# Optimization experiments

Hardware: AMD Instinct MI355X
Metric: run time of the kernel (lower is better)

The kernel has to match this reference:

```python
import jax, jax.numpy as jnp
import numpy as np

H = 8          # n_heads
THRESH = 0.5   # edge pruning threshold
LN_EPS = 1e-5


def setup_inputs() -> dict:
    key = jax.random.key(0)
    ks = jax.random.split(key, 24)
    B, S, D = 8, 128, 256
    N = S + 1
    hd = D // H

    def lin(k, fan_in, fan_out, gain=1.0):
        # xavier_uniform-ish init, stored as [in, out] (y = x @ W + b)
        lim = gain * np.sqrt(6.0 / (fan_in + fan_out))
        return jax.random.uniform(k, (fan_in, fan_out), jnp.float32, -lim, lim)

    g = 1.0 / np.sqrt(2.0)
    return {
        "desc": jax.random.normal(ks[0], (B, S, D), jnp.float32),
        "nv": jax.random.normal(ks[1], (B, N, D), jnp.float32),
        "W_gt": lin(ks[2], D, D), "b_gt": jnp.zeros((D,), jnp.float32),
        "topo_bias": jnp.zeros((1,), jnp.float32),
        "W_q": lin(ks[3], D, D, g), "b_q": jnp.zeros((D,), jnp.float32),
        "W_k": lin(ks[4], D, D, g), "b_k": jnp.zeros((D,), jnp.float32),
        "W_v": lin(ks[5], D, D, g), "b_v": jnp.zeros((D,), jnp.float32),
        "W_e1": lin(ks[6], 2 * D, D), "b_e1": jnp.zeros((D,), jnp.float32),
        "ln_g": jnp.ones((D,), jnp.float32), "ln_b": jnp.zeros((D,), jnp.float32),
        "W_e2": lin(ks[7], D, D), "b_e2": jnp.zeros((D,), jnp.float32),
        "w_attn": lin(ks[8], 3 * hd, 1, g)[:, 0], "b_attn": jnp.zeros((), jnp.float32),
        "W_o": lin(ks[9], D, D, g), "b_o": jnp.zeros((D,), jnp.float32),
    }


def _forward(desc, nv, W_gt, b_gt, topo_bias, W_q, b_q, W_k, b_k, W_v, b_v,
             W_e1, b_e1, ln_g, ln_b, W_e2, b_e2, w_attn, b_attn, W_o, b_o):
    B, N, D = nv.shape
    S = N - 1
    hd = D // H

    # 1. global topology
    d = desc @ W_gt + b_gt                                   # [B,S,D]
    dn = d / jnp.linalg.norm(d, axis=-1, keepdims=True)
    global_top = jax.nn.sigmoid(jnp.einsum('bid,bjd->bij', dn, dn) + topo_bias[0])

    # 2. sample-wise similarity
    var = nv[:, 1:, :]
    vn = var / jnp.linalg.norm(var, axis=-1, keepdims=True)
    sample_sim = jnp.einsum('bid,bjd->bij', vn, vn)
    adj_mat = global_top * sample_sim

    # 3. remove self-connection, squash
    diag_mask = 1.0 - jnp.eye(S, dtype=adj_mat.dtype)
    adj = jax.nn.sigmoid(adj_mat * diag_mask)

    # 4. straight-through edge pruning (frozen=False path)
    hard = (adj > THRESH).astype(adj.dtype)
    adj = hard - jax.lax.stop_gradient(adj) + adj

    # 5. edge attributes: Linear(concat(d_i,d_j)) decomposed into two matmuls
    a = d @ W_e1[:D]                                          # node_i part [B,S,D]
    b_ = d @ W_e1[D:]                                         # node_j part [B,S,D]
    pre = jnp.zeros((B, N, N, D), dtype=d.dtype)
    pre = pre.at[:, 1:, 1:].set(a[:, :, None, :] + b_[:, None, :, :])
    cls = a + b_                                              # concat(d_j,d_j) rows
    pre = pre.at[:, 0, 1:].set(cls).at[:, 1:, 0].set(cls)
    pre = pre + b_e1                                          # (0,0) entry = bias only (zeros input)
    mu = pre.mean(-1, keepdims=True)
    vr = ((pre - mu) ** 2).mean(-1, keepdims=True)
    e = jax.nn.relu((pre - mu) * jax.lax.rsqrt(vr + LN_EPS) * ln_g + ln_b)
    e = e @ W_e2 + b_e2                                       # [B,N,N,D]
    e = e.reshape(B, N, N, H, hd).transpose(0, 3, 1, 2, 4)    # [B,H,N,N,hd]

    # padded adjacency: CLS row attends to all vars, col 0 masked
    na = jnp.zeros((B, N, N), dtype=adj.dtype)
    na = na.at[:, 1:, 1:].set(adj).at[:, 0, 1:].set(1.0)
    e = e * na[:, None, :, :, None]

    # 6. additive attention: attn_proj(concat(q,k,e)) decomposed
    q = (nv @ W_q + b_q).reshape(B, N, H, hd).transpose(0, 2, 1, 3)
    k = (nv @ W_k + b_k).reshape(B, N, H, hd).transpose(0, 2, 1, 3)
    v = (nv @ W_v + b_v).reshape(B, N, H, hd).transpose(0, 2, 1, 3)
    wq, wk, we = w_attn[:hd], w_attn[hd:2 * hd], w_attn[2 * hd:]
    scores = (jnp.einsum('bhid,d->bhi', q, wq)[:, :, :, None]
              + jnp.einsum('bhjd,d->bhj', k, wk)[:, :, None, :]
              + jnp.einsum('bhijd,d->bhij', e, we) + b_attn)
    scores = scores + (na[:, None, :, :] == 0).astype(scores.dtype) * -1e9
    attn = jax.nn.softmax(scores, axis=-1)                    # dropout = identity (eval)

    ctx = jnp.einsum('bhij,bhjd->bhid', attn, v)
    out = ctx.transpose(0, 2, 1, 3).reshape(B, N, D) @ W_o + b_o
    return out, attn


def reference(desc, nv, W_gt, b_gt, topo_bias, W_q, b_q, W_k, b_k, W_v, b_v,
              W_e1, b_e1, ln_g, ln_b, W_e2, b_e2, w_attn, b_attn, W_o, b_o):
    return _forward(desc, nv, W_gt, b_gt, topo_bias, W_q, b_q, W_k, b_k, W_v, b_v,
                    W_e1, b_e1, ln_g, ln_b, W_e2, b_e2, w_attn, b_attn, W_o, b_o)
```

## Files before the change

kernel.cpp:

```cpp
#include <hip/hip_runtime.h>
#include <math.h>

#define BB 8
#define SS 128
#define NN 129
#define DD 256
#define HH 8
#define LN_EPS 1e-5f

#define OFF_A    0
#define OFF_BPT  262144
#define OFF_CPT  524288
#define OFF_VART 786432
#define OFF_V    1048576
#define OFF_SQ   1312768
#define OFF_SK   1321024
#define OFF_MA   1329280
#define OFF_QA   1330304
#define OFF_MB   1331328
#define OFF_QB   1332352
#define OFF_MC   1333376
#define OFF_QC   1334400
#define OFF_U    1335424
#define OFF_UB   1337472

struct SA {
    float dsc[4][DD];
    float drow[4][DD];
    float4 red[8][4][64];
    float part[24][4];
};
struct SB {
    float rows[2][DD];
    float4 redq[8][2][64];
    float4 redk[8][2][64];
};
union SMA { SA a; SB b; };

__global__ __launch_bounds__(512) void ka_all(
    const float* __restrict__ desc, const float* __restrict__ nv,
    const float* __restrict__ W_gt, const float* __restrict__ b_gt,
    const float* __restrict__ W_e1, const float* __restrict__ b_e1,
    const float* __restrict__ W_q, const float* __restrict__ b_q,
    const float* __restrict__ W_k, const float* __restrict__ b_k,
    const float* __restrict__ W_v, const float* __restrict__ b_v,
    const float* __restrict__ W_e2, const float* __restrict__ b_e2,
    const float* __restrict__ w_attn,
    float* __restrict__ a, float* __restrict__ bp_t, float* __restrict__ cp_t,
    float* __restrict__ var_t, float* __restrict__ v,
    float* __restrict__ sq, float* __restrict__ sk,
    float* __restrict__ ma, float* __restrict__ qa, float* __restrict__ mb,
    float* __restrict__ qb, float* __restrict__ mc, float* __restrict__ qc,
    float* __restrict__ U, float* __restrict__ ubias) {
    __shared__ SMA sm;
    const int bx = blockIdx.x, t = threadIdx.x;

    if (bx < 256) {
        SA& S = sm.a;
        const int b = bx >> 5, s0 = (bx & 31) * 4;
        const int dq = t & 63, kh = t >> 6;
        for (int e = t; e < 4 * DD; e += 512)
            S.dsc[e >> 8][e & 255] = desc[(size_t)(b * SS + s0 + (e >> 8)) * DD + (e & 255)];
        __syncthreads();
        {
            float4 acc[4];
#pragma unroll
            for (int r = 0; r < 4; r++) acc[r] = make_float4(0.f, 0.f, 0.f, 0.f);
            const int kb = kh * 32;
#pragma unroll 4
            for (int k = kb; k < kb + 32; k++) {
                float4 w = *(const float4*)&W_gt[k * DD + 4 * dq];
#pragma unroll
                for (int r = 0; r < 4; r++) {
                    float x = S.dsc[r][k];
                    acc[r].x = fmaf(x, w.x, acc[r].x); acc[r].y = fmaf(x, w.y, acc[r].y);
                    acc[r].z = fmaf(x, w.z, acc[r].z); acc[r].w = fmaf(x, w.w, acc[r].w);
                }
            }
#pragma unroll
            for (int r = 0; r < 4; r++) S.red[kh][r][dq] = acc[r];
        }
        __syncthreads();
        for (int e = t; e < 4 * DD; e += 512) {
            int r = e >> 8, d2 = e & 255;
            float s = b_gt[d2];
#pragma unroll
            for (int kk = 0; kk < 8; kk++) s += ((const float*)S.red[kk][r])[d2];
            S.drow[r][d2] = s;
        }
        __syncthreads();
        {
            float4 acc[4];
#pragma unroll
            for (int r = 0; r < 4; r++) acc[r] = make_float4(0.f, 0.f, 0.f, 0.f);
            const int kb = kh * 32;
#pragma unroll 4
            for (int k = kb; k < kb + 32; k++) {
                float4 w = *(const float4*)&W_e1[k * DD + 4 * dq];
#pragma unroll
                for (int r = 0; r < 4; r++) {
                    float x = S.drow[r][k];
                    acc[r].x = fmaf(x, w.x, acc[r].x); acc[r].y = fmaf(x, w.y, acc[r].y);
                    acc[r].z = fmaf(x, w.z, acc[r].z); acc[r].w = fmaf(x, w.w, acc[r].w);
                }
            }
#pragma unroll
            for (int r = 0; r < 4; r++) S.red[kh][r][dq] = acc[r];
        }
        __syncthreads();
        float avf[4];
        if (t < 256) {
            const int d2 = t;
#pragma unroll
            for (int r = 0; r < 4; r++) {
                float s = 0.f;
#pragma unroll
                for (int kk = 0; kk < 8; kk++) s += ((const float*)S.red[kk][r])[d2];
                avf[r] = s;
                a[(size_t)(b * SS + s0 + r) * DD + d2] = s;
            }
        }
        __syncthreads();
        {
            float4 acc[4];
#pragma unroll
            for (int r = 0; r < 4; r++) acc[r] = make_float4(0.f, 0.f, 0.f, 0.f);
            const int kb = kh * 32;
#pragma unroll 4
            for (int k = kb; k < kb + 32; k++) {
                float4 w = *(const float4*)&W_e1[(DD + k) * DD + 4 * dq];
#pragma unroll
                for (int r = 0; r < 4; r++) {
                    float x = S.drow[r][k];
                    acc[r].x = fmaf(x, w.x, acc[r].x); acc[r].y = fmaf(x, w.y, acc[r].y);
                    acc[r].z = fmaf(x, w.z, acc[r].z); acc[r].w = fmaf(x, w.w, acc[r].w);
                }
            }
#pragma unroll
            for (int r = 0; r < 4; r++) S.red[kh][r][dq] = acc[r];
        }
        __syncthreads();
        if (t < 256) {
            const int d2 = t;
            float bvf[4], cvf[4];
            float be1 = b_e1[d2];
#pragma unroll
            for (int r = 0; r < 4; r++) {
                float s = 0.f;
#pragma unroll
                for (int kk = 0; kk < 8; kk++) s += ((const float*)S.red[kk][r])[d2];
                bvf[r] = s + be1; cvf[r] = avf[r] + bvf[r];
            }
            float4 f4;
            f4.x = bvf[0]; f4.y = bvf[1]; f4.z = bvf[2]; f4.w = bvf[3];
            *(float4*)(bp_t + (size_t)(b * DD + d2) * SS + s0) = f4;
            f4.x = cvf[0]; f4.y = cvf[1]; f4.z = cvf[2]; f4.w = cvf[3];
            *(float4*)(cp_t + (size_t)(b * DD + d2) * SS + s0) = f4;
            float nvv[4];
#pragma unroll
            for (int r = 0; r < 4; r++) nvv[r] = nv[(size_t)(b * NN + 1 + s0 + r) * DD + d2];
            f4.x = nvv[0]; f4.y = nvv[1]; f4.z = nvv[2]; f4.w = nvv[3];
            *(float4*)(var_t + (size_t)(b * DD + d2) * SS + s0) = f4;
            float vals[24];
#pragma unroll
            for (int r = 0; r < 4; r++) {
                vals[r * 6 + 0] = avf[r]; vals[r * 6 + 1] = avf[r] * avf[r];
                vals[r * 6 + 2] = bvf[r]; vals[r * 6 + 3] = bvf[r] * bvf[r];
                vals[r * 6 + 4] = cvf[r]; vals[r * 6 + 5] = cvf[r] * cvf[r];
            }
            int lane = t & 63, wid = t >> 6;
#pragma unroll
            for (int vv = 0; vv < 24; vv++) {
                float x = vals[vv];
                for (int o = 32; o; o >>= 1) x += __shfl_xor(x, o, 64);
                if (lane == 0) S.part[vv][wid] = x;
            }
        }
        __syncthreads();
        if (t < 24) {
            float ssum = (S.part[t][0] + S.part[t][1]) + (S.part[t][2] + S.part[t][3]);
            int st = t % 6;
            int row = b * SS + s0 + t / 6;
            float m = ssum * (1.f / DD);
            float* dstp = (st == 0) ? ma : (st == 1) ? qa : (st == 2) ? mb
                         : (st == 3) ? qb : (st == 4) ? mc : qc;
            dstp[row] = m;
        }
    } else if (bx < 776) {
        SB& S = sm.b;
        const int idx = bx - 256;
        const int b = idx / 65, n0 = (idx % 65) * 2;
        const int dq = t & 63, kh = t >> 6;
        if (t < 512) {
            int r = t >> 8, d2 = t & 255;
            int n = n0 + r; if (n >= NN) n = NN - 1;
            S.rows[r][d2] = nv[(size_t)(b * NN + n) * DD + d2];
        }
        __syncthreads();
        {
            float4 aq[2], ak[2];
#pragma unroll
            for (int r = 0; r < 2; r++) { aq[r] = make_float4(0.f, 0.f, 0.f, 0.f); ak[r] = aq[r]; }
            const int kb = kh * 32;
#pragma unroll 4
            for (int k = kb; k < kb + 32; k++) {
                float4 wq = *(const float4*)&W_q[k * DD + 4 * dq];
                float4 wk = *(const float4*)&W_k[k * DD + 4 * dq];
#pragma unroll
                for (int r = 0; r < 2; r++) {
                    float x = S.rows[r][k];
                    aq[r].x = fmaf(x, wq.x, aq[r].x); aq[r].y = fmaf(x, wq.y, aq[r].y);
                    aq[r].z = fmaf(x, wq.z, aq[r].z); aq[r].w = fmaf(x, wq.w, aq[r].w);
                    ak[r].x = fmaf(x, wk.x, ak[r].x); ak[r].y = fmaf(x, wk.y, ak[r].y);
                    ak[r].z = fmaf(x, wk.z, ak[r].z); ak[r].w = fmaf(x, wk.w, ak[r].w);
                }
            }
#pragma unroll
            for (int r = 0; r < 2; r++) { S.redq[kh][r][dq] = aq[r]; S.redk[kh][r][dq] = ak[r]; }
        }
        __syncthreads();
        {
            const int d2 = t & 255, r = t >> 8;
            const int n = n0 + r;
            float qf = b_q[d2], kf = b_k[d2];
#pragma unroll
            for (int kk = 0; kk < 8; kk++) {
                qf += ((const float*)S.redq[kk][r])[d2];
                kf += ((const float*)S.redk[kk][r])[d2];
            }
            float xq = qf * w_attn[d2 & 31];
            float xk = kf * w_attn[32 + (d2 & 31)];
#pragma unroll
            for (int o = 16; o; o >>= 1) { xq += __shfl_xor(xq, o, 32); xk += __shfl_xor(xk, o, 32); }
            if ((d2 & 31) == 0 && n < NN) {
                sq[(size_t)(b * HH + (d2 >> 5)) * NN + n] = xq;
                sk[(size_t)(b * HH + (d2 >> 5)) * NN + n] = xk;
            }
        }
        __syncthreads();
        {
            float4 av[2];
#pragma unroll
            for (int r = 0; r < 2; r++) av[r] = make_float4(0.f, 0.f, 0.f, 0.f);
            const int kb = kh * 32;
#pragma unroll 4
            for (int k = kb; k < kb + 32; k++) {
                float4 wv = *(const float4*)&W_v[k * DD + 4 * dq];
#pragma unroll
                for (int r = 0; r < 2; r++) {
                    float x = S.rows[r][k];
                    av[r].x = fmaf(x, wv.x, av[r].x); av[r].y = fmaf(x, wv.y, av[r].y);
                    av[r].z = fmaf(x, wv.z, av[r].z); av[r].w = fmaf(x, wv.w, av[r].w);
                }
            }
#pragma unroll
            for (int r = 0; r < 2; r++) S.redq[kh][r][dq] = av[r];
        }
        __syncthreads();
        {
            const int d2 = t & 255, r = t >> 8;
            const int n = n0 + r;
            if (n < NN) {
                float vf = b_v[d2];
#pragma unroll
                for (int kk = 0; kk < 8; kk++) vf += ((const float*)S.redq[kk][r])[d2];
                v[(size_t)(b * NN + n) * DD + d2] = vf;
            }
        }
    } else {
        const int ri = bx - 776;
        if (t < 256) {
            const int c = t;
            const float wec = w_attn[64 + (c & 31)];
#pragma unroll
            for (int rr = 0; rr < 4; rr++) {
                int r = ri * 4 + rr;
                float x = W_e2[(size_t)r * DD + c] * wec;
#pragma unroll
                for (int o = 16; o; o >>= 1) x += __shfl_xor(x, o, 32);
                if ((c & 31) == 0) U[r * HH + (c >> 5)] = x;
            }
            if (ri == 0) {
                float x = b_e2[c] * wec;
#pragma unroll
                for (int o = 16; o; o >>= 1) x += __shfl_xor(x, o, 32);
                if ((c & 31) == 0) ubias[c >> 5] = x;
            }
        }
    }
}

__global__ __launch_bounds__(256) void kb_scores(
    const float* __restrict__ a, const float* __restrict__ bp_t, const float* __restrict__ cp_t,
    const float* __restrict__ var_t, const float* __restrict__ nv,
    const float* __restrict__ ma, const float* __restrict__ qa,
    const float* __restrict__ mb, const float* __restrict__ qb,
    const float* __restrict__ mc, const float* __restrict__ qc,
    const float* __restrict__ sq, const float* __restrict__ sk,
    const float* __restrict__ ln_g, const float* __restrict__ ln_b,
    const float* __restrict__ U, const float* __restrict__ ubias,
    const float* __restrict__ b_attn,
    float* __restrict__ attn) {
    const int i = blockIdx.x, b = blockIdx.y;
    const int t = threadIdx.x, j = t & 127, dh = t >> 7;
    __shared__ float Arow[DD];
    __shared__ float Vrow[DD];
    __shared__ float2 lnsm[DD];
    __shared__ __attribute__((aligned(16))) float4 Usm[DD][2];
    __shared__ float skm[HH * NN];
    __shared__ float sc[HH][132];
    __shared__ float accred[128][9];
    __shared__ float redc[128][2];
    __shared__ float redv[128][2];

    Arow[t] = (i >= 1) ? a[((size_t)b * SS + i - 1) * DD + t] : 0.f;
    Vrow[t] = nv[((size_t)b * NN + i) * DD + t];
    { float2 g; g.x = ln_g[t]; g.y = ln_b[t]; lnsm[t] = g; }
    Usm[t][0] = *(const float4*)&U[t * HH];
    Usm[t][1] = *(const float4*)&U[t * HH + 4];
    for (int e = t; e < HH * NN; e += 256) skm[e] = sk[(size_t)b * (HH * NN) + e];
    __syncthreads();

    float cr = 0.f, dv = 0.f;
    if (i >= 1) {
        const float* bc = bp_t + ((size_t)b * DD + dh * 128) * SS;
        const float* vc = var_t + ((size_t)b * DD + dh * 128) * SS;
#pragma unroll 8
        for (int dd = 0; dd < 128; dd++) {
            float Bv = bc[(size_t)dd * SS + j];
            float Vv = vc[(size_t)dd * SS + j];
            cr = fmaf(Arow[dh * 128 + dd], Bv, cr);
            dv = fmaf(Vrow[dh * 128 + dd], Vv, dv);
        }
    }
    redc[j][dh] = cr; redv[j][dh] = dv;
    __syncthreads();
    cr = redc[j][0] + redc[j][1];
    dv = redv[j][0] + redv[j][1];
    float rs, nm, mk, pen;
    if (i == 0) {
        float mu = mc[b * SS + j], q2 = qc[b * SS + j];
        rs = rsqrtf(q2 - mu * mu + LN_EPS); nm = -mu * rs; mk = 1.f; pen = 0.f;
    } else {
        float muA = ma[b * SS + i - 1], qA = qa[b * SS + i - 1];
        float muB = mb[b * SS + j],     qB = qb[b * SS + j];
        float mu = muA + muB;
        float var = qA + qB + 2.f * cr * (1.f / DD) - mu * mu;
        rs = rsqrtf(var + LN_EPS); nm = -mu * rs;
        mk = ((i - 1) != j && dv > 0.f) ? 1.f : 0.f;
        pen = (mk == 0.f) ? -1e9f : 0.f;
    }

    float acc[HH];
#pragma unroll
    for (int h = 0; h < HH; h++) acc[h] = 0.f;
    {
        const float* Bp = ((i == 0) ? cp_t : bp_t) + ((size_t)b * DD + dh * 128) * SS;
#pragma unroll 4
        for (int dd = 0; dd < 128; dd++) {
            const int d2 = dh * 128 + dd;
            float Bv = Bp[(size_t)dd * SS + j];
            float pre = Arow[d2] + Bv;
            float y = fmaf(pre, rs, nm);
            float2 gb = lnsm[d2];
            y = fmaf(y, gb.x, gb.y);
            float rr = fmaxf(y, 0.f);
            float4 u0 = Usm[d2][0], u1 = Usm[d2][1];
            acc[0] = fmaf(rr, u0.x, acc[0]); acc[1] = fmaf(rr, u0.y, acc[1]);
            acc[2] = fmaf(rr, u0.z, acc[2]); acc[3] = fmaf(rr, u0.w, acc[3]);
            acc[4] = fmaf(rr, u1.x, acc[4]); acc[5] = fmaf(rr, u1.y, acc[5]);
            acc[6] = fmaf(rr, u1.z, acc[6]); acc[7] = fmaf(rr, u1.w, acc[7]);
        }
    }
    if (dh == 1) {
#pragma unroll
        for (int h = 0; h < HH; h++) accred[j][h] = acc[h];
    }
    __syncthreads();
    if (dh == 0) {
        const float ba = b_attn[0];
#pragma unroll
        for (int h = 0; h < HH; h++) {
            float af = acc[h] + accred[j][h];
            float sqv = sq[(size_t)b * (HH * NN) + h * NN + i];
            sc[h][1 + j] = sqv + skm[h * NN + 1 + j] + (af + ubias[h]) * mk + ba + pen;
        }
        if (j == 0) {
#pragma unroll
            for (int h = 0; h < HH; h++)
                sc[h][0] = sq[(size_t)b * (HH * NN) + h * NN + i] + skm[h * NN] + ba - 1e9f;
        }
    }
    __syncthreads();

    {
        const int h = t >> 5, l = t & 31;
        float m = -INFINITY;
        for (int jj = l; jj < NN; jj += 32) m = fmaxf(m, sc[h][jj]);
#pragma unroll
        for (int o = 16; o; o >>= 1) m = fmaxf(m, __shfl_xor(m, o, 32));
        float s = 0.f;
        for (int jj = l; jj < NN; jj += 32) { float e = __expf(sc[h][jj] - m); sc[h][jj] = e; s += e; }
#pragma unroll
        for (int o = 16; o; o >>= 1) s += __shfl_xor(s, o, 32);
        float inv = 1.f / s;
        float* arow = attn + (((size_t)b * HH + h) * NN + i) * NN;
        for (int jj = l; jj < NN; jj += 32) arow[jj] = sc[h][jj] * inv;
    }
}

__global__ __launch_bounds__(512) void kc_out(
    const float* __restrict__ attn, const float* __restrict__ v,
    const float* __restrict__ W_o, const float* __restrict__ b_o,
    float* __restrict__ out) {
    const int b = blockIdx.y, i0 = blockIdx.x * 4;
    const int t = threadIdx.x;
    __shared__ float ar[4][HH * 133];
    __shared__ float red[2][4][DD];
    __shared__ float csm[4][DD];
    for (int e = t; e < 4 * HH * NN; e += 512) {
        int il = e / (HH * NN), r = e - il * (HH * NN);
        int h = r / NN, jj = r - h * NN;
        int i = i0 + il; if (i > NN - 1) i = NN - 1;
        ar[il][h * 133 + jj] = attn[(((size_t)b * HH + h) * NN + i) * NN + jj];
    }
    __syncthreads();
    {
        const int d = t & 255, jh = t >> 8;
        const int h = d >> 5;
        float cacc[4] = {0.f, 0.f, 0.f, 0.f};
        const int j0 = jh * 65, j1 = (jh == 0) ? 65 : NN;
        for (int jj = j0; jj < j1; jj++) {
            float vv = v[((size_t)b * NN + jj) * DD + d];
            cacc[0] = fmaf(ar[0][h * 133 + jj], vv, cacc[0]);
            cacc[1] = fmaf(ar[1][h * 133 + jj], vv, cacc[1]);
            cacc[2] = fmaf(ar[2][h * 133 + jj], vv, cacc[2]);
            cacc[3] = fmaf(ar[3][h * 133 + jj], vv, cacc[3]);
        }
#pragma unroll
        for (int il = 0; il < 4; il++) red[jh][il][d] = cacc[il];
    }
    __syncthreads();
    for (int e = t; e < 4 * DD; e += 512) {
        int il = e >> 8, d = e & 255;
        csm[il][d] = red[0][il][d] + red[1][il][d];
    }
    __syncthreads();
    {
        const int d2 = t & 255, kh = t >> 8;
        float o[4] = {0.f, 0.f, 0.f, 0.f};
        const int kb = kh * 128;
#pragma unroll 8
        for (int k = kb; k < kb + 128; k++) {
            float w = W_o[(size_t)k * DD + d2];
            o[0] = fmaf(csm[0][k], w, o[0]); o[1] = fmaf(csm[1][k], w, o[1]);
            o[2] = fmaf(csm[2][k], w, o[2]); o[3] = fmaf(csm[3][k], w, o[3]);
        }
#pragma unroll
        for (int il = 0; il < 4; il++) red[kh][il][d2] = o[il];
    }
    __syncthreads();
    for (int e = t; e < 4 * DD; e += 512) {
        int il = e >> 8, d = e & 255;
        int i = i0 + il;
        if (i < NN)
            out[((size_t)b * NN + i) * DD + d] = red[0][il][d] + red[1][il][d] + b_o[d];
    }
}

extern "C" void kernel_launch(void* const* d_in, const int* in_sizes, int n_in,
                              void* d_out, int out_size, void* d_ws, size_t ws_size,
                              hipStream_t stream) {
    const float* desc   = (const float*)d_in[0];
    const float* nv     = (const float*)d_in[1];
    const float* W_gt   = (const float*)d_in[2];
    const float* b_gt   = (const float*)d_in[3];
    const float* W_q    = (const float*)d_in[5];
    const float* b_q    = (const float*)d_in[6];
    const float* W_k    = (const float*)d_in[7];
    const float* b_k    = (const float*)d_in[8];
    const float* W_v    = (const float*)d_in[9];
    const float* b_v    = (const float*)d_in[10];
    const float* W_e1   = (const float*)d_in[11];
    const float* b_e1   = (const float*)d_in[12];
    const float* ln_g   = (const float*)d_in[13];
    const float* ln_b   = (const float*)d_in[14];
    const float* W_e2   = (const float*)d_in[15];
    const float* b_e2   = (const float*)d_in[16];
    const float* w_attn = (const float*)d_in[17];
    const float* b_attn = (const float*)d_in[18];
    const float* W_o    = (const float*)d_in[19];
    const float* b_o    = (const float*)d_in[20];

    float* ws   = (float*)d_ws;
    float* a    = ws + OFF_A;
    float* bp_t = ws + OFF_BPT;
    float* cp_t = ws + OFF_CPT;
    float* vart = ws + OFF_VART;
    float* v    = ws + OFF_V;
    float* sq   = ws + OFF_SQ;
    float* sk   = ws + OFF_SK;
    float* ma   = ws + OFF_MA;
    float* qa   = ws + OFF_QA;
    float* mb   = ws + OFF_MB;
    float* qb   = ws + OFF_QB;
    float* mc   = ws + OFF_MC;
    float* qc   = ws + OFF_QC;
    float* U    = ws + OFF_U;
    float* ub   = ws + OFF_UB;

    float* out  = (float*)d_out;
    float* attn = (float*)d_out + (size_t)BB * NN * DD;

    ka_all<<<dim3(840), dim3(512), 0, stream>>>(
        desc, nv, W_gt, b_gt, W_e1, b_e1, W_q, b_q, W_k, b_k, W_v, b_v,
        W_e2, b_e2, w_attn,
        a, bp_t, cp_t, vart, v, sq, sk, ma, qa, mb, qb, mc, qc, U, ub);
    kb_scores<<<dim3(NN, BB), dim3(256), 0, stream>>>(
        a, bp_t, cp_t, vart, nv, ma, qa, mb, qb, mc, qc, sq, sk,
        ln_g, ln_b, U, ub, b_attn, attn);
    kc_out<<<dim3((NN + 3) / 4, BB), dim3(512), 0, stream>>>(attn, v, W_o, b_o, out);
}
```

Before: 189.8 us.

## Rewrite all three kernels with per-thread full-K columns and register-tiled scores

All three kernels are restructured around 256-thread blocks. In the projection kernel each thread owns one output column over the full K range, which removes the split-K shared-memory reductions and their barriers, and Q/K/V and both W_e1 halves are now computed in a single fused pass. The scores kernel now gives each thread four j columns across a 32-wide d slice, loading B as float4 and precomputing per-j LayerNorm stats into shared memory, followed by an 8-way shared reduction. The output kernel handles 2 rows per block instead of 4, giving more blocks but less reuse of W_o and v.

Result: no change. 191.2 us (+0.7%).

```diff
diff --git a/kernel.cpp b/kernel.cpp
--- a/kernel.cpp
+++ b/kernel.cpp
@@ -24,20 +24,7 @@
 #define OFF_U    1335424
 #define OFF_UB   1337472
 
-struct SA {
-    float dsc[4][DD];
-    float drow[4][DD];
-    float4 red[8][4][64];
-    float part[24][4];
-};
-struct SB {
-    float rows[2][DD];
-    float4 redq[8][2][64];
-    float4 redk[8][2][64];
-};
-union SMA { SA a; SB b; };
-
-__global__ __launch_bounds__(512) void ka_all(
+__global__ __launch_bounds__(256) void ka2(
     const float* __restrict__ desc, const float* __restrict__ nv,
     const float* __restrict__ W_gt, const float* __restrict__ b_gt,
     const float* __restrict__ W_e1, const float* __restrict__ b_e1,
@@ -52,133 +39,77 @@
     float* __restrict__ ma, float* __restrict__ qa, float* __restrict__ mb,
     float* __restrict__ qb, float* __restrict__ mc, float* __restrict__ qc,
     float* __restrict__ U, float* __restrict__ ubias) {
-    __shared__ SMA sm;
     const int bx = blockIdx.x, t = threadIdx.x;
+    __shared__ __attribute__((aligned(16))) float rowbuf[DD][4];
+    __shared__ __attribute__((aligned(16))) float drow[DD][4];
+    __shared__ float part[24][4];
 
     if (bx < 256) {
-        SA& S = sm.a;
         const int b = bx >> 5, s0 = (bx & 31) * 4;
-        const int dq = t & 63, kh = t >> 6;
-        for (int e = t; e < 4 * DD; e += 512)
-            S.dsc[e >> 8][e & 255] = desc[(size_t)(b * SS + s0 + (e >> 8)) * DD + (e & 255)];
+        for (int e = t; e < 4 * DD; e += 256) {
+            int r = e >> 8, k = e & 255;
+            rowbuf[k][r] = desc[(size_t)(b * SS + s0 + r) * DD + k];
+        }
         __syncthreads();
+        const int c = t;
         {
-            float4 acc[4];
-#pragma unroll
-            for (int r = 0; r < 4; r++) acc[r] = make_float4(0.f, 0.f, 0.f, 0.f);
-            const int kb = kh * 32;
+            float dv[4] = {0.f, 0.f, 0.f, 0.f};
+#pragma unroll 8
+            for (int k = 0; k < DD; k++) {
+                float w = W_gt[k * DD + c];
+                float4 d4 = *(const float4*)&rowbuf[k][0];
+                dv[0] = fmaf(d4.x, w, dv[0]); dv[1] = fmaf(d4.y, w, dv[1]);
+                dv[2] = fmaf(d4.z, w, dv[2]); dv[3] = fmaf(d4.w, w, dv[3]);
+            }
+            float bg = b_gt[c];
+            float4 st; st.x = dv[0] + bg; st.y = dv[1] + bg; st.z = dv[2] + bg; st.w = dv[3] + bg;
+            *(float4*)&drow[c][0] = st;
+        }
+        __syncthreads();
+        float av[4] = {0.f, 0.f, 0.f, 0.f}, bv[4] = {0.f, 0.f, 0.f, 0.f};
 #pragma unroll 4
-            for (int k = kb; k < kb + 32; k++) {
-                float4 w = *(const float4*)&W_gt[k * DD + 4 * dq];
-#pragma unroll
-                for (int r = 0; r < 4; r++) {
-                    float x = S.dsc[r][k];
-                    acc[r].x = fmaf(x, w.x, acc[r].x); acc[r].y = fmaf(x, w.y, acc[r].y);
-                    acc[r].z = fmaf(x, w.z, acc[r].z); acc[r].w = fmaf(x, w.w, acc[r].w);
-                }
-            }
-#pragma unroll
-            for (int r = 0; r < 4; r++) S.red[kh][r][dq] = acc[r];
-        }
-        __syncthreads();
-        for (int e = t; e < 4 * DD; e += 512) {
-            int r = e >> 8, d2 = e & 255;
-            float s = b_gt[d2];
-#pragma unroll
-            for (int kk = 0; kk < 8; kk++) s += ((const float*)S.red[kk][r])[d2];
-            S.drow[r][d2] = s;
-        }
-        __syncthreads();
-        {
-            float4 acc[4];
-#pragma unroll
-            for (int r = 0; r < 4; r++) acc[r] = make_float4(0.f, 0.f, 0.f, 0.f);
-            const int kb = kh * 32;
-#pragma unroll 4
-            for (int k = kb; k < kb + 32; k++) {
-                float4 w = *(const float4*)&W_e1[k * DD + 4 * dq];
-#pragma unroll
-                for (int r = 0; r < 4; r++) {
-                    float x = S.drow[r][k];
-                    acc[r].x = fmaf(x, w.x, acc[r].x); acc[r].y = fmaf(x, w.y, acc[r].y);
-                    acc[r].z = fmaf(x, w.z, acc[r].z); acc[r].w = fmaf(x, w.w, acc[r].w);
-                }
-            }
-#pragma unroll
-            for (int r = 0; r < 4; r++) S.red[kh][r][dq] = acc[r];
-        }
-        __syncthreads();
-        float avf[4];
-        if (t < 256) {
-            const int d2 = t;
-#pragma unroll
-            for (int r = 0; r < 4; r++) {
-                float s = 0.f;
-#pragma unroll
-                for (int kk = 0; kk < 8; kk++) s += ((const float*)S.red[kk][r])[d2];
-                avf[r] = s;
-                a[(size_t)(b * SS + s0 + r) * DD + d2] = s;
-            }
-        }
-        __syncthreads();
-        {
-            float4 acc[4];
-#pragma unroll
-            for (int r = 0; r < 4; r++) acc[r] = make_float4(0.f, 0.f, 0.f, 0.f);
-            const int kb = kh * 32;
-#pragma unroll 4
-            for (int k = kb; k < kb + 32; k++) {
-                float4 w = *(const float4*)&W_e1[(DD + k) * DD + 4 * dq];
-#pragma unroll
-                for (int r = 0; r < 4; r++) {
-                    float x = S.drow[r][k];
-                    acc[r].x = fmaf(x, w.x, acc[r].x); acc[r].y = fmaf(x, w.y, acc[r].y);
-                    acc[r].z = fmaf(x, w.z, acc[r].z); acc[r].w = fmaf(x, w.w, acc[r].w);
-                }
-            }
-#pragma unroll
-            for (int r = 0; r < 4; r++) S.red[kh][r][dq] = acc[r];
-        }
-        __syncthreads();
-        if (t < 256) {
-            const int d2 = t;
-            float bvf[4], cvf[4];
-            float be1 = b_e1[d2];
-#pragma unroll
-            for (int r = 0; r < 4; r++) {
-                float s = 0.f;
-#pragma unroll
-                for (int kk = 0; kk < 8; kk++) s += ((const float*)S.red[kk][r])[d2];
-                bvf[r] = s + be1; cvf[r] = avf[r] + bvf[r];
-            }
-            float4 f4;
-            f4.x = bvf[0]; f4.y = bvf[1]; f4.z = bvf[2]; f4.w = bvf[3];
-            *(float4*)(bp_t + (size_t)(b * DD + d2) * SS + s0) = f4;
-            f4.x = cvf[0]; f4.y = cvf[1]; f4.z = cvf[2]; f4.w = cvf[3];
-            *(float4*)(cp_t + (size_t)(b * DD + d2) * SS + s0) = f4;
-            float nvv[4];
-#pragma unroll
-            for (int r = 0; r < 4; r++) nvv[r] = nv[(size_t)(b * NN + 1 + s0 + r) * DD + d2];
-            f4.x = nvv[0]; f4.y = nvv[1]; f4.z = nvv[2]; f4.w = nvv[3];
-            *(float4*)(var_t + (size_t)(b * DD + d2) * SS + s0) = f4;
-            float vals[24];
-#pragma unroll
-            for (int r = 0; r < 4; r++) {
-                vals[r * 6 + 0] = avf[r]; vals[r * 6 + 1] = avf[r] * avf[r];
-                vals[r * 6 + 2] = bvf[r]; vals[r * 6 + 3] = bvf[r] * bvf[r];
-                vals[r * 6 + 4] = cvf[r]; vals[r * 6 + 5] = cvf[r] * cvf[r];
-            }
-            int lane = t & 63, wid = t >> 6;
-#pragma unroll
-            for (int vv = 0; vv < 24; vv++) {
-                float x = vals[vv];
-                for (int o = 32; o; o >>= 1) x += __shfl_xor(x, o, 64);
-                if (lane == 0) S.part[vv][wid] = x;
-            }
+        for (int k = 0; k < DD; k++) {
+            float wa = W_e1[k * DD + c];
+            float wb = W_e1[(DD + k) * DD + c];
+            float4 d4 = *(const float4*)&drow[k][0];
+            av[0] = fmaf(d4.x, wa, av[0]); av[1] = fmaf(d4.y, wa, av[1]);
+            av[2] = fmaf(d4.z, wa, av[2]); av[3] = fmaf(d4.w, wa, av[3]);
+            bv[0] = fmaf(d4.x, wb, bv[0]); bv[1] = fmaf(d4.y, wb, bv[1]);
+            bv[2] = fmaf(d4.z, wb, bv[2]); bv[3] = fmaf(d4.w, wb, bv[3]);
+        }
+        float be1 = b_e1[c];
+        float cv[4];
+#pragma unroll
+        for (int r = 0; r < 4; r++) { bv[r] += be1; cv[r] = av[r] + bv[r]; }
+#pragma unroll
+        for (int r = 0; r < 4; r++) a[(size_t)(b * SS + s0 + r) * DD + c] = av[r];
+        float4 f4;
+        f4.x = bv[0]; f4.y = bv[1]; f4.z = bv[2]; f4.w = bv[3];
+        *(float4*)(bp_t + (size_t)(b * DD + c) * SS + s0) = f4;
+        f4.x = cv[0]; f4.y = cv[1]; f4.z = cv[2]; f4.w = cv[3];
+        *(float4*)(cp_t + (size_t)(b * DD + c) * SS + s0) = f4;
+        float nvv[4];
+#pragma unroll
+        for (int r = 0; r < 4; r++) nvv[r] = nv[(size_t)(b * NN + 1 + s0 + r) * DD + c];
+        f4.x = nvv[0]; f4.y = nvv[1]; f4.z = nvv[2]; f4.w = nvv[3];
+        *(float4*)(var_t + (size_t)(b * DD + c) * SS + s0) = f4;
+        float vals[24];
+#pragma unroll
+        for (int r = 0; r < 4; r++) {
+            vals[r * 6 + 0] = av[r]; vals[r * 6 + 1] = av[r] * av[r];
+            vals[r * 6 + 2] = bv[r]; vals[r * 6 + 3] = bv[r] * bv[r];
+            vals[r * 6 + 4] = cv[r]; vals[r * 6 + 5] = cv[r] * cv[r];
+        }
+        int lane = t & 63, wid = t >> 6;
+#pragma unroll
+        for (int vv = 0; vv < 24; vv++) {
+            float x = vals[vv];
+            for (int o = 32; o; o >>= 1) x += __shfl_xor(x, o, 64);
+            if (lane == 0) part[vv][wid] = x;
         }
         __syncthreads();
         if (t < 24) {
-            float ssum = (S.part[t][0] + S.part[t][1]) + (S.part[t][2] + S.part[t][3]);
+            float ssum = (part[t][0] + part[t][1]) + (part[t][2] + part[t][3]);
             int st = t % 6;
             int row = b * SS + s0 + t / 6;
             float m = ssum * (1.f / DD);
@@ -186,111 +117,67 @@
                          : (st == 3) ? qb : (st == 4) ? mc : qc;
             dstp[row] = m;
         }
-    } else if (bx < 776) {
-        SB& S = sm.b;
+    } else if (bx < 520) {
         const int idx = bx - 256;
-        const int b = idx / 65, n0 = (idx % 65) * 2;
-        const int dq = t & 63, kh = t >> 6;
-        if (t < 512) {
-            int r = t >> 8, d2 = t & 255;
+        const int b = idx / 33, n0 = (idx % 33) * 4;
+        for (int e = t; e < 4 * DD; e += 256) {
+            int r = e >> 8, k = e & 255;
             int n = n0 + r; if (n >= NN) n = NN - 1;
-            S.rows[r][d2] = nv[(size_t)(b * NN + n) * DD + d2];
+            rowbuf[k][r] = nv[(size_t)(b * NN + n) * DD + k];
         }
         __syncthreads();
-        {
-            float4 aq[2], ak[2];
-#pragma unroll
-            for (int r = 0; r < 2; r++) { aq[r] = make_float4(0.f, 0.f, 0.f, 0.f); ak[r] = aq[r]; }
-            const int kb = kh * 32;
+        const int c = t;
+        float qv[4] = {0.f, 0.f, 0.f, 0.f}, kv[4] = {0.f, 0.f, 0.f, 0.f},
+              vv[4] = {0.f, 0.f, 0.f, 0.f};
 #pragma unroll 4
-            for (int k = kb; k < kb + 32; k++) {
-                float4 wq = *(const float4*)&W_q[k * DD + 4 * dq];
-                float4 wk = *(const float4*)&W_k[k * DD + 4 * dq];
-#pragma unroll
-                for (int r = 0; r < 2; r++) {
-                    float x = S.rows[r][k];
-                    aq[r].x = fmaf(x, wq.x, aq[r].x); aq[r].y = fmaf(x, wq.y, aq[r].y);
-                    aq[r].z = fmaf(x, wq.z, aq[r].z); aq[r].w = fmaf(x, wq.w, aq[r].w);
-                    ak[r].x = fmaf(x, wk.x, ak[r].x); ak[r].y = fmaf(x, wk.y, ak[r].y);
-                    ak[r].z = fmaf(x, wk.z, ak[r].z); ak[r].w = fmaf(x, wk.w, ak[r].w);
-                }
+        for (int k = 0; k < DD; k++) {
+            float wq = W_q[k * DD + c], wk = W_k[k * DD + c], wvv = W_v[k * DD + c];
+            float4 r4 = *(const float4*)&rowbuf[k][0];
+            qv[0] = fmaf(r4.x, wq, qv[0]); qv[1] = fmaf(r4.y, wq, qv[1]);
+            qv[2] = fmaf(r4.z, wq, qv[2]); qv[3] = fmaf(r4.w, wq, qv[3]);
+            kv[0] = fmaf(r4.x, wk, kv[0]); kv[1] = fmaf(r4.y, wk, kv[1]);
+            kv[2] = fmaf(r4.z, wk, kv[2]); kv[3] = fmaf(r4.w, wk, kv[3]);
+            vv[0] = fmaf(r4.x, wvv, vv[0]); vv[1] = fmaf(r4.y, wvv, vv[1]);
+            vv[2] = fmaf(r4.z, wvv, vv[2]); vv[3] = fmaf(r4.w, wvv, vv[3]);
+        }
+        float bq = b_q[c], bk = b_k[c], bvb = b_v[c];
+        float waq = w_attn[c & 31];
+        float wak = w_attn[32 + (c & 31)];
+        int h = c >> 5;
+#pragma unroll
+        for (int r = 0; r < 4; r++) {
+            int n = n0 + r;
+            if (n < NN) v[(size_t)(b * NN + n) * DD + c] = vv[r] + bvb;
+            float xq = (qv[r] + bq) * waq, xk = (kv[r] + bk) * wak;
+#pragma unroll
+            for (int o = 16; o; o >>= 1) { xq += __shfl_xor(xq, o); xk += __shfl_xor(xk, o); }
+            if ((c & 31) == 0 && n < NN) {
+                sq[(size_t)(b * HH + h) * NN + n] = xq;
+                sk[(size_t)(b * HH + h) * NN + n] = xk;
             }
-#pragma unroll
-            for (int r = 0; r < 2; r++) { S.redq[kh][r][dq] = aq[r]; S.redk[kh][r][dq] = ak[r]; }
-        }
-        __syncthreads();
-        {
-            const int d2 = t & 255, r = t >> 8;
-            const int n = n0 + r;
-            float qf = b_q[d2], kf = b_k[d2];
-#pragma unroll
-            for (int kk = 0; kk < 8; kk++) {
-                qf += ((const float*)S.redq[kk][r])[d2];
-                kf += ((const float*)S.redk[kk][r])[d2];
-            }
-            float xq = qf * w_attn[d2 & 31];
-            float xk = kf * w_attn[32 + (d2 & 31)];
-#pragma unroll
-            for (int o = 16; o; o >>= 1) { xq += __shfl_xor(xq, o, 32); xk += __shfl_xor(xk, o, 32); }
-            if ((d2 & 31) == 0 && n < NN) {
-                sq[(size_t)(b * HH + (d2 >> 5)) * NN + n] = xq;
-                sk[(size_t)(b * HH + (d2 >> 5)) * NN + n] = xk;
-            }
-        }
-        __syncthreads();
-        {
-            float4 av[2];
-#pragma unroll
-            for (int r = 0; r < 2; r++) av[r] = make_float4(0.f, 0.f, 0.f, 0.f);
-            const int kb = kh * 32;
-#pragma unroll 4
-            for (int k = kb; k < kb + 32; k++) {
-                float4 wv = *(const float4*)&W_v[k * DD + 4 * dq];
-#pragma unroll
-                for (int r = 0; r < 2; r++) {
-                    float x = S.rows[r][k];
-                    av[r].x = fmaf(x, wv.x, av[r].x); av[r].y = fmaf(x, wv.y, av[r].y);
-                    av[r].z = fmaf(x, wv.z, av[r].z); av[r].w = fmaf(x, wv.w, av[r].w);
-                }
-            }
-#pragma unroll
-            for (int r = 0; r < 2; r++) S.redq[kh][r][dq] = av[r];
-        }
-        __syncthreads();
-        {
-            const int d2 = t & 255, r = t >> 8;
-            const int n = n0 + r;
-            if (n < NN) {
-                float vf = b_v[d2];
-#pragma unroll
-                for (int kk = 0; kk < 8; kk++) vf += ((const float*)S.redq[kk][r])[d2];
-                v[(size_t)(b * NN + n) * DD + d2] = vf;
-            }
         }
     } else {
-        const int ri = bx - 776;
-        if (t < 256) {
-            const int c = t;
-            const float wec = w_attn[64 + (c & 31)];
-#pragma unroll
-            for (int rr = 0; rr < 4; rr++) {
-                int r = ri * 4 + rr;
-                float x = W_e2[(size_t)r * DD + c] * wec;
-#pragma unroll
-                for (int o = 16; o; o >>= 1) x += __shfl_xor(x, o, 32);
-                if ((c & 31) == 0) U[r * HH + (c >> 5)] = x;
-            }
-            if (ri == 0) {
-                float x = b_e2[c] * wec;
-#pragma unroll
-                for (int o = 16; o; o >>= 1) x += __shfl_xor(x, o, 32);
-                if ((c & 31) == 0) ubias[c >> 5] = x;
-            }
+        const int ri = bx - 520;
+        const int c = t;
+        const float wec = w_attn[64 + (c & 31)];
+#pragma unroll
+        for (int rr = 0; rr < 4; rr++) {
+            int r = ri * 4 + rr;
+            float x = W_e2[(size_t)r * DD + c] * wec;
+#pragma unroll
+            for (int o = 16; o; o >>= 1) x += __shfl_xor(x, o);
+            if ((c & 31) == 0) U[r * HH + (c >> 5)] = x;
+        }
+        if (ri == 0) {
+            float x = b_e2[c] * wec;
+#pragma unroll
+            for (int o = 16; o; o >>= 1) x += __shfl_xor(x, o);
+            if ((c & 31) == 0) ubias[c >> 5] = x;
         }
     }
 }
 
-__global__ __launch_bounds__(256) void kb_scores(
+__global__ __launch_bounds__(256) void kb2(
     const float* __restrict__ a, const float* __restrict__ bp_t, const float* __restrict__ cp_t,
     const float* __restrict__ var_t, const float* __restrict__ nv,
     const float* __restrict__ ma, const float* __restrict__ qa,
@@ -302,95 +189,124 @@
     const float* __restrict__ b_attn,
     float* __restrict__ attn) {
     const int i = blockIdx.x, b = blockIdx.y;
-    const int t = threadIdx.x, j = t & 127, dh = t >> 7;
+    const int t = threadIdx.x, jq = t & 31, dg = t >> 5;
     __shared__ float Arow[DD];
     __shared__ float Vrow[DD];
     __shared__ float2 lnsm[DD];
     __shared__ __attribute__((aligned(16))) float4 Usm[DD][2];
-    __shared__ float skm[HH * NN];
+    __shared__ __attribute__((aligned(16))) float rsm[SS], nmm[SS], mkm[SS], pnm[SS];
+    __shared__ float sqb[HH], ubm[HH];
     __shared__ float sc[HH][132];
-    __shared__ float accred[128][9];
-    __shared__ float redc[128][2];
-    __shared__ float redv[128][2];
+    __shared__ __attribute__((aligned(16))) float red[8][HH * SS];
 
     Arow[t] = (i >= 1) ? a[((size_t)b * SS + i - 1) * DD + t] : 0.f;
     Vrow[t] = nv[((size_t)b * NN + i) * DD + t];
     { float2 g; g.x = ln_g[t]; g.y = ln_b[t]; lnsm[t] = g; }
     Usm[t][0] = *(const float4*)&U[t * HH];
     Usm[t][1] = *(const float4*)&U[t * HH + 4];
-    for (int e = t; e < HH * NN; e += 256) skm[e] = sk[(size_t)b * (HH * NN) + e];
-    __syncthreads();
-
-    float cr = 0.f, dv = 0.f;
+    if (t < HH) {
+        sqb[t] = sq[(size_t)b * HH * NN + t * NN + i] + b_attn[0];
+        ubm[t] = ubias[t];
+    }
+    __syncthreads();
+
     if (i >= 1) {
-        const float* bc = bp_t + ((size_t)b * DD + dh * 128) * SS;
-        const float* vc = var_t + ((size_t)b * DD + dh * 128) * SS;
+        float cr[4] = {0.f, 0.f, 0.f, 0.f}, dv[4] = {0.f, 0.f, 0.f, 0.f};
+        const float* bc = bp_t + ((size_t)b * DD + dg * 32) * SS + 4 * jq;
+        const float* vc = var_t + ((size_t)b * DD + dg * 32) * SS + 4 * jq;
 #pragma unroll 8
-        for (int dd = 0; dd < 128; dd++) {
-            float Bv = bc[(size_t)dd * SS + j];
-            float Vv = vc[(size_t)dd * SS + j];
-            cr = fmaf(Arow[dh * 128 + dd], Bv, cr);
-            dv = fmaf(Vrow[dh * 128 + dd], Vv, dv);
-        }
-    }
-    redc[j][dh] = cr; redv[j][dh] = dv;
-    __syncthreads();
-    cr = redc[j][0] + redc[j][1];
-    dv = redv[j][0] + redv[j][1];
-    float rs, nm, mk, pen;
-    if (i == 0) {
-        float mu = mc[b * SS + j], q2 = qc[b * SS + j];
-        rs = rsqrtf(q2 - mu * mu + LN_EPS); nm = -mu * rs; mk = 1.f; pen = 0.f;
-    } else {
-        float muA = ma[b * SS + i - 1], qA = qa[b * SS + i - 1];
-        float muB = mb[b * SS + j],     qB = qb[b * SS + j];
-        float mu = muA + muB;
-        float var = qA + qB + 2.f * cr * (1.f / DD) - mu * mu;
-        rs = rsqrtf(var + LN_EPS); nm = -mu * rs;
-        mk = ((i - 1) != j && dv > 0.f) ? 1.f : 0.f;
-        pen = (mk == 0.f) ? -1e9f : 0.f;
-    }
-
-    float acc[HH];
-#pragma unroll
-    for (int h = 0; h < HH; h++) acc[h] = 0.f;
+        for (int dd = 0; dd < 32; dd++) {
+            float4 b4 = *(const float4*)(bc + (size_t)dd * SS);
+            float4 v4 = *(const float4*)(vc + (size_t)dd * SS);
+            float A = Arow[dg * 32 + dd], V = Vrow[dg * 32 + dd];
+            cr[0] = fmaf(A, b4.x, cr[0]); cr[1] = fmaf(A, b4.y, cr[1]);
+            cr[2] = fmaf(A, b4.z, cr[2]); cr[3] = fmaf(A, b4.w, cr[3]);
+            dv[0] = fmaf(V, v4.x, dv[0]); dv[1] = fmaf(V, v4.y, dv[1]);
+            dv[2] = fmaf(V, v4.z, dv[2]); dv[3] = fmaf(V, v4.w, dv[3]);
+        }
+        float4 s0; s0.x = cr[0]; s0.y = cr[1]; s0.z = cr[2]; s0.w = cr[3];
+        float4 s1; s1.x = dv[0]; s1.y = dv[1]; s1.z = dv[2]; s1.w = dv[3];
+        *(float4*)&red[dg][4 * jq] = s0;
+        *(float4*)&red[dg][SS + 4 * jq] = s1;
+    }
+    __syncthreads();
+    if (t < SS) {
+        const int j = t;
+        float rs, nm, mk, pen;
+        if (i == 0) {
+            float mu = mc[b * SS + j], q2 = qc[b * SS + j];
+            rs = rsqrtf(q2 - mu * mu + LN_EPS); nm = -mu * rs; mk = 1.f; pen = 0.f;
+        } else {
+            float cr = 0.f, dv = 0.f;
+#pragma unroll
+            for (int g = 0; g < 8; g++) { cr += red[g][j]; dv += red[g][SS + j]; }
+            float muA = ma[b * SS + i - 1], qA = qa[b * SS + i - 1];
+            float muB = mb[b * SS + j], qB = qb[b * SS + j];
+            float mu = muA + muB;
+            float var = qA + qB + 2.f * cr * (1.f / DD) - mu * mu;
+            rs = rsqrtf(var + LN_EPS); nm = -mu * rs;
+            mk = ((i - 1) != j && dv > 0.f) ? 1.f : 0.f;
+            pen = (mk == 0.f) ? -1e9f : 0.f;
+        }
+        rsm[j] = rs; nmm[j] = nm; mkm[j] = mk; pnm[j] = pen;
+    }
+    __syncthreads();
+
+    float acc[4][HH];
+#pragma unroll
+    for (int jj = 0; jj < 4; jj++)
+#pragma unroll
+        for (int h = 0; h < HH; h++) acc[jj][h] = 0.f;
     {
-        const float* Bp = ((i == 0) ? cp_t : bp_t) + ((size_t)b * DD + dh * 128) * SS;
+        const float* Bp = ((i == 0) ? cp_t : bp_t) + ((size_t)b * DD + dg * 32) * SS + 4 * jq;
+        float4 rs4 = *(const float4*)&rsm[4 * jq];
+        float4 nm4 = *(const float4*)&nmm[4 * jq];
+        float rsv[4] = {rs4.x, rs4.y, rs4.z, rs4.w};
+        float nmv[4] = {nm4.x, nm4.y, nm4.z, nm4.w};
 #pragma unroll 4
-        for (int dd = 0; dd < 128; dd++) {
-            const int d2 = dh * 128 + dd;
-            float Bv = Bp[(size_t)dd * SS + j];
-            float pre = Arow[d2] + Bv;
-            float y = fmaf(pre, rs, nm);
+        for (int dd = 0; dd < 32; dd++) {
+            const int d2 = dg * 32 + dd;
+            float4 b4 = *(const float4*)(Bp + (size_t)dd * SS);
+            float A = Arow[d2];
             float2 gb = lnsm[d2];
-            y = fmaf(y, gb.x, gb.y);
-            float rr = fmaxf(y, 0.f);
             float4 u0 = Usm[d2][0], u1 = Usm[d2][1];
-            acc[0] = fmaf(rr, u0.x, acc[0]); acc[1] = fmaf(rr, u0.y, acc[1]);
-            acc[2] = fmaf(rr, u0.z, acc[2]); acc[3] = fmaf(rr, u0.w, acc[3]);
-            acc[4] = fmaf(rr, u1.x, acc[4]); acc[5] = fmaf(rr, u1.y, acc[5]);
-            acc[6] = fmaf(rr, u1.z, acc[6]); acc[7] = fmaf(rr, u1.w, acc[7]);
-        }
-    }
-    if (dh == 1) {
-#pragma unroll
-        for (int h = 0; h < HH; h++) accred[j][h] = acc[h];
-    }
-    __syncthreads();
-    if (dh == 0) {
-        const float ba = b_attn[0];
-#pragma unroll
-        for (int h = 0; h < HH; h++) {
-            float af = acc[h] + accred[j][h];
-            float sqv = sq[(size_t)b * (HH * NN) + h * NN + i];
-            sc[h][1 + j] = sqv + skm[h * NN + 1 + j] + (af + ubias[h]) * mk + ba + pen;
-        }
-        if (j == 0) {
-#pragma unroll
-            for (int h = 0; h < HH; h++)
-                sc[h][0] = sq[(size_t)b * (HH * NN) + h * NN + i] + skm[h * NN] + ba - 1e9f;
-        }
-    }
+            float bj[4] = {b4.x, b4.y, b4.z, b4.w};
+#pragma unroll
+            for (int jj = 0; jj < 4; jj++) {
+                float y = fmaf(A + bj[jj], rsv[jj], nmv[jj]);
+                y = fmaf(y, gb.x, gb.y);
+                float rr = fmaxf(y, 0.f);
+                acc[jj][0] = fmaf(rr, u0.x, acc[jj][0]);
+                acc[jj][1] = fmaf(rr, u0.y, acc[jj][1]);
+                acc[jj][2] = fmaf(rr, u0.z, acc[jj][2]);
+                acc[jj][3] = fmaf(rr, u0.w, acc[jj][3]);
+                acc[jj][4] = fmaf(rr, u1.x, acc[jj][4]);
+                acc[jj][5] = fmaf(rr, u1.y, acc[jj][5]);
+                acc[jj][6] = fmaf(rr, u1.z, acc[jj][6]);
+                acc[jj][7] = fmaf(rr, u1.w, acc[jj][7]);
+            }
+        }
+    }
+#pragma unroll
+    for (int h = 0; h < HH; h++) {
+        float4 w4;
+        w4.x = acc[0][h]; w4.y = acc[1][h]; w4.z = acc[2][h]; w4.w = acc[3][h];
+        *(float4*)&red[dg][h * SS + 4 * jq] = w4;
+    }
+    __syncthreads();
+    {
+        const int j = t >> 1, hb = (t & 1) * 4;
+#pragma unroll
+        for (int hh = 0; hh < 4; hh++) {
+            int h = hb + hh;
+            float s = 0.f;
+#pragma unroll
+            for (int g = 0; g < 8; g++) s += red[g][h * SS + j];
+            float skv = sk[(size_t)b * HH * NN + h * NN + 1 + j];
+            sc[h][1 + j] = sqb[h] + skv + (s + ubm[h]) * mkm[j] + pnm[j];
+        }
+    }
+    if (t < HH) sc[t][0] = sqb[t] + sk[(size_t)b * HH * NN + t * NN] - 1e9f;
     __syncthreads();
 
     {
@@ -398,73 +314,57 @@
         float m = -INFINITY;
         for (int jj = l; jj < NN; jj += 32) m = fmaxf(m, sc[h][jj]);
 #pragma unroll
-        for (int o = 16; o; o >>= 1) m = fmaxf(m, __shfl_xor(m, o, 32));
+        for (int o = 16; o; o >>= 1) m = fmaxf(m, __shfl_xor(m, o));
         float s = 0.f;
         for (int jj = l; jj < NN; jj += 32) { float e = __expf(sc[h][jj] - m); sc[h][jj] = e; s += e; }
 #pragma unroll
-        for (int o = 16; o; o >>= 1) s += __shfl_xor(s, o, 32);
+        for (int o = 16; o; o >>= 1) s += __shfl_xor(s, o);
         float inv = 1.f / s;
         float* arow = attn + (((size_t)b * HH + h) * NN + i) * NN;
         for (int jj = l; jj < NN; jj += 32) arow[jj] = sc[h][jj] * inv;
     }
 }
 
-__global__ __launch_bounds__(512) void kc_out(
+__global__ __launch_bounds__(256) void kc2(
     const float* __restrict__ attn, const float* __restrict__ v,
     const float* __restrict__ W_o, const float* __restrict__ b_o,
     float* __restrict__ out) {
-    const int b = blockIdx.y, i0 = blockIdx.x * 4;
+    const int b = blockIdx.y, i0 = blockIdx.x * 2;
     const int t = threadIdx.x;
-    __shared__ float ar[4][HH * 133];
-    __shared__ float red[2][4][DD];
-    __shared__ float csm[4][DD];
-    for (int e = t; e < 4 * HH * NN; e += 512) {
+    __shared__ float ar[2][HH * 132];
+    __shared__ __attribute__((aligned(8))) float csm[DD][2];
+    for (int e = t; e < 2 * HH * NN; e += 256) {
         int il = e / (HH * NN), r = e - il * (HH * NN);
-        int h = r / NN, jj = r - h * NN;
-        int i = i0 + il; if (i > NN - 1) i = NN - 1;
-        ar[il][h * 133 + jj] = attn[(((size_t)b * HH + h) * NN + i) * NN + jj];
+        int h = r / NN, j = r - h * NN;
+        int i = i0 + il; if (i >= NN) i = NN - 1;
+        ar[il][h * 132 + j] = attn[(((size_t)b * HH + h) * NN + i) * NN + j];
     }
     __syncthreads();
     {
-        const int d = t & 255, jh = t >> 8;
-        const int h = d >> 5;
-        float cacc[4] = {0.f, 0.f, 0.f, 0.f};
-        const int j0 = jh * 65, j1 = (jh == 0) ? 65 : NN;
-        for (int jj = j0; jj < j1; jj++) {
-            float vv = v[((size_t)b * NN + jj) * DD + d];
-            cacc[0] = fmaf(ar[0][h * 133 + jj], vv, cacc[0]);
-            cacc[1] = fmaf(ar[1][h * 133 + jj], vv, cacc[1]);
-            cacc[2] = fmaf(ar[2][h * 133 + jj], vv, cacc[2]);
-            cacc[3] = fmaf(ar[3][h * 133 + jj], vv, cacc[3]);
-        }
-#pragma unroll
-        for (int il = 0; il < 4; il++) red[jh][il][d] = cacc[il];
-    }
-    __syncthreads();
-    for (int e = t; e < 4 * DD; e += 512) {
-        int il = e >> 8, d = e & 255;
-        csm[il][d] = red[0][il][d] + red[1][il][d];
+        const int d = t, h = d >> 5;
+        float c0 = 0.f, c1 = 0.f;
+        const float* vp = v + (size_t)b * NN * DD + d;
+#pragma unroll 4
+        for (int j = 0; j < NN; j++) {
+            float vv = vp[(size_t)j * DD];
+            c0 = fmaf(ar[0][h * 132 + j], vv, c0);
+            c1 = fmaf(ar[1][h * 132 + j], vv, c1);
+        }
+        csm[d][0] = c0; csm[d][1] = c1;
     }
     __syncthreads();
     {
-        const int d2 = t & 255, kh = t >> 8;
-        float o[4] = {0.f, 0.f, 0.f, 0.f};
-        const int kb = kh * 128;
+        const int c = t;
+        float o0 = 0.f, o1 = 0.f;
 #pragma unroll 8
-        for (int k = kb; k < kb + 128; k++) {
-            float w = W_o[(size_t)k * DD + d2];
-            o[0] = fmaf(csm[0][k], w, o[0]); o[1] = fmaf(csm[1][k], w, o[1]);
-            o[2] = fmaf(csm[2][k], w, o[2]); o[3] = fmaf(csm[3][k], w, o[3]);
-        }
-#pragma unroll
-        for (int il = 0; il < 4; il++) red[kh][il][d2] = o[il];
-    }
-    __syncthreads();
-    for (int e = t; e < 4 * DD; e += 512) {
-        int il = e >> 8, d = e & 255;
-        int i = i0 + il;
-        if (i < NN)
-            out[((size_t)b * NN + i) * DD + d] = red[0][il][d] + red[1][il][d] + b_o[d];
+        for (int k = 0; k < DD; k++) {
+            float w = W_o[(size_t)k * DD + c];
+            float2 cv = *(const float2*)&csm[k][0];
+            o0 = fmaf(cv.x, w, o0); o1 = fmaf(cv.y, w, o1);
+        }
+        float bo = b_o[c];
+        out[((size_t)b * NN + i0) * DD + c] = o0 + bo;
+        if (i0 + 1 < NN) out[((size_t)b * NN + i0 + 1) * DD + c] = o1 + bo;
     }
 }
 
@@ -512,12 +412,12 @@
     float* out  = (float*)d_out;
     float* attn = (float*)d_out + (size_t)BB * NN * DD;
 
-    ka_all<<<dim3(840), dim3(512), 0, stream>>>(
+    ka2<<<dim3(584), dim3(256), 0, stream>>>(
         desc, nv, W_gt, b_gt, W_e1, b_e1, W_q, b_q, W_k, b_k, W_v, b_v,
         W_e2, b_e2, w_attn,
         a, bp_t, cp_t, vart, v, sq, sk, ma, qa, mb, qb, mc, qc, U, ub);
-    kb_scores<<<dim3(NN, BB), dim3(256), 0, stream>>>(
+    kb2<<<dim3(NN, BB), dim3(256), 0, stream>>>(
         a, bp_t, cp_t, vart, nv, ma, qa, mb, qb, mc, qc, sq, sk,
         ln_g, ln_b, U, ub, b_attn, attn);
-    kc_out<<<dim3((NN + 3) / 4, BB), dim3(512), 0, stream>>>(attn, v, W_o, b_o, out);
+    kc2<<<dim3((NN + 1) / 2, BB), dim3(256), 0, stream>>>(attn, v, W_o, b_o, out);
 }
```
